# Kernel tuning notes

Hardware: AMD Instinct MI355X
Metric: run time of the kernel (lower is better)

Reference implementation:

```python
import jax, jax.numpy as jnp
import numpy as np

B, T, C = 2, 2048, 2048
N_HEAD = 16

def setup_inputs() -> dict:
    key = jax.random.key(0)
    k1, k2, k3 = jax.random.split(key, 3)
    scale = 1.0 / np.sqrt(C)
    return {
        "x": jax.random.normal(k1, (B, T, C), dtype=jnp.float32),
        "w_attn": jax.random.normal(k2, (C, 3 * C), dtype=jnp.float32) * scale,
        "b_attn": jnp.zeros((3 * C,), dtype=jnp.float32),
        "w_proj": jax.random.normal(k3, (C, C), dtype=jnp.float32) * scale,
        "b_proj": jnp.zeros((C,), dtype=jnp.float32),
    }

def reference(x, w_attn, b_attn, w_proj, b_proj):
    Bb, Tt, Cc = x.shape
    hd = Cc // N_HEAD  # head_size
    qkv = x @ w_attn + b_attn              # [B,T,3C]
    q, k, v = jnp.split(qkv, 3, axis=-1)
    # [B,T,C] -> [B,H,T,hd]
    def heads(t):
        return t.reshape(Bb, Tt, N_HEAD, hd).transpose(0, 2, 1, 3)
    q, k, v = heads(q), heads(k), heads(v)
    att = jnp.einsum("bhqd,bhkd->bhqk", q, k) * (hd ** -0.5)
    causal = jnp.tril(jnp.ones((Tt, Tt), dtype=bool))
    att = jnp.where(causal[None, None], att, -jnp.inf)
    att = jax.nn.softmax(att, axis=-1)
    out = jnp.einsum("bhqk,bhkd->bhqd", att, v)
    out = out.transpose(0, 2, 1, 3).reshape(Bb, Tt, Cc)
    return out @ w_proj + b_proj
```

## Files before the change

kernel.cpp:

```cpp
#include <hip/hip_runtime.h>
#include <cstdint>
#include <cstddef>

typedef __bf16 bf16_t;
typedef __bf16 bf16x8 __attribute__((ext_vector_type(8)));
typedef __bf16 bf16x4 __attribute__((ext_vector_type(4)));
typedef float floatx4 __attribute__((ext_vector_type(4)));
typedef float f32x16 __attribute__((ext_vector_type(16)));

#define B_  2
#define T_  2048
#define C_  2048
#define H_  16
#define HD_ 128

#define K_ATTN_SCALE (0.08838834764831843f * 1.44269504088896f)

__device__ __forceinline__ void async_copy16(const void* g, void* l) {
  __builtin_amdgcn_global_load_lds((const __attribute__((address_space(1))) unsigned int*)g,
                                   (__attribute__((address_space(3))) unsigned int*)l,
                                   16, 0, 0);
}

#define BAR()     asm volatile("s_barrier" ::: "memory")
#define VMCNT(n)  asm volatile("s_waitcnt vmcnt(" #n ")" ::: "memory")

__global__ __launch_bounds__(256) void cvt_f32_bf16(const float* __restrict__ in,
                                                    bf16_t* __restrict__ out, int n4) {
  int i = blockIdx.x * 256 + threadIdx.x;
  if (i >= n4) return;
  const float4 v = ((const float4*)in)[i];
  bf16x4 o;
  o[0] = (bf16_t)v.x; o[1] = (bf16_t)v.y; o[2] = (bf16_t)v.z; o[3] = (bf16_t)v.w;
  ((bf16x4*)out)[i] = o;
}

__global__ __launch_bounds__(256) void transpose_cvt(const float* __restrict__ W,
                                                     bf16_t* __restrict__ Wt,
                                                     int Kd, int Nd) {
  __shared__ float tile[32][33];
  const int tx = threadIdx.x, ty = threadIdx.y;
  const int n0 = blockIdx.x * 32, k0 = blockIdx.y * 32;
#pragma unroll
  for (int j = ty; j < 32; j += 8)
    tile[j][tx] = W[(size_t)(k0 + j) * Nd + n0 + tx];
  __syncthreads();
#pragma unroll
  for (int j = ty; j < 32; j += 8)
    Wt[(size_t)(n0 + j) * Kd + k0 + tx] = (bf16_t)tile[tx][j];
}

#define GBM 256
#define GBN 256
#define GBK 64

__global__ __launch_bounds__(512, 2) void gemm_qkv(
    const bf16_t* __restrict__ A, const bf16_t* __restrict__ Bt,
    const float* __restrict__ bias,
    bf16_t* __restrict__ Qo, bf16_t* __restrict__ Ko, bf16_t* __restrict__ Vo,
    int K) {
  __shared__ __align__(16) char smem[131072];
  const int tid = threadIdx.x;
  const int wave = tid >> 6, lane = tid & 63;
  const int quad = lane >> 4, l15 = lane & 15;
  const int wm = wave >> 2, wn = wave & 3;
  const int bm = blockIdx.y * GBM, bn = blockIdx.x * GBN;

  const bf16_t* asrc[2];
  const bf16_t* bsrc[2];
#pragma unroll
  for (int l = 0; l < 2; ++l) {
    int p = l * 8192 + tid * 16;
    int r = p >> 6;
    int c = ((p >> 4) & 3) ^ ((r >> 1) & 3);
    asrc[l] = A  + (size_t)(bm + r) * K + c * 8;
    bsrc[l] = Bt + (size_t)(bn + r) * K + c * 8;
  }

  auto stage = [&](int buf, int ks, int kofs) {
    char* Asl = smem + buf * 65536 + ks * 16384;
    char* Bsl = Asl + 32768;
#pragma unroll
    for (int l = 0; l < 2; ++l)
      async_copy16(asrc[l] + kofs, Asl + l * 8192 + tid * 16);
#pragma unroll
    for (int l = 0; l < 2; ++l)
      async_copy16(bsrc[l] + kofs, Bsl + l * 8192 + tid * 16);
  };

  const int sxr = ((l15 >> 1) & 3) << 4;
  const int cb  = (quad * 16) ^ sxr;
  const int arow = (wm * 128 + l15) * 64;
  const int brow = (wn * 64 + l15) * 64;

  floatx4 acc[8][4] = {};
  bf16x8 a0[4], a1[4], b0[4], b1[4];

  stage(0, 0, 0);
  stage(0, 1, 32);
  stage(1, 0, GBK);
  VMCNT(8);
  BAR();
  {
    const char* Ab = smem;
    const char* Bb = smem + 32768;
#pragma unroll
    for (int i = 0; i < 4; ++i)
      a0[i] = *(const bf16x8*)(Ab + arow + i * 1024 + cb);
#pragma unroll
    for (int j = 0; j < 4; ++j)
      b0[j] = *(const bf16x8*)(Bb + brow + j * 1024 + cb);
  }

  const int NT = K / GBK;
  for (int t = 0; t < NT; ++t) {
    const char* Ab  = smem + (t & 1) * 65536;
    const char* Bb  = Ab + 32768;
    const char* Abn = smem + ((t + 1) & 1) * 65536;
    const char* Bbn = Abn + 32768;

#pragma unroll
    for (int i = 0; i < 4; ++i)
      a1[i] = *(const bf16x8*)(Ab + arow + 4096 + i * 1024 + cb);
    if (t + 1 < NT) stage((t + 1) & 1, 1, (t + 1) * GBK + 32);
#pragma unroll
    for (int i = 0; i < 4; ++i)
#pragma unroll
      for (int j = 0; j < 4; ++j)
        acc[i][j] = __builtin_amdgcn_mfma_f32_16x16x32_bf16(a0[i], b0[j], acc[i][j], 0, 0, 0);
    if (t + 1 < NT) { VMCNT(8); } else { VMCNT(0); }
    BAR();

#pragma unroll
    for (int i = 0; i < 4; ++i)
      a0[i] = *(const bf16x8*)(Ab + 16384 + arow + i * 1024 + cb);
#pragma unroll
    for (int j = 0; j < 4; ++j)
      b1[j] = *(const bf16x8*)(Bb + 16384 + brow + j * 1024 + cb);
#pragma unroll
    for (int i = 0; i < 4; ++i)
#pragma unroll
      for (int j = 0; j < 4; ++j)
        acc[4 + i][j] = __builtin_amdgcn_mfma_f32_16x16x32_bf16(a1[i], b0[j], acc[4 + i][j], 0, 0, 0);

#pragma unroll
    for (int i = 0; i < 4; ++i)
      a1[i] = *(const bf16x8*)(Ab + 16384 + arow + 4096 + i * 1024 + cb);
    if (t + 2 < NT) stage(t & 1, 0, (t + 2) * GBK);
#pragma unroll
    for (int i = 0; i < 4; ++i)
#pragma unroll
      for (int j = 0; j < 4; ++j)
        acc[i][j] = __builtin_amdgcn_mfma_f32_16x16x32_bf16(a0[i], b1[j], acc[i][j], 0, 0, 0);
    if (t + 2 < NT)      { VMCNT(8); }
    else if (t + 1 < NT) { VMCNT(4); }
    else                 { VMCNT(0); }
    BAR();

    if (t + 1 < NT) {
#pragma unroll
      for (int i = 0; i < 4; ++i)
        a0[i] = *(const bf16x8*)(Abn + arow + i * 1024 + cb);
#pragma unroll
      for (int j = 0; j < 4; ++j)
        b0[j] = *(const bf16x8*)(Bbn + brow + j * 1024 + cb);
    }
#pragma unroll
    for (int i = 0; i < 4; ++i)
#pragma unroll
      for (int j = 0; j < 4; ++j)
        acc[4 + i][j] = __builtin_amdgcn_mfma_f32_16x16x32_bf16(a1[i], b1[j], acc[4 + i][j], 0, 0, 0);
  }

  float bias_r[4];
#pragma unroll
  for (int j = 0; j < 4; ++j)
    bias_r[j] = bias[bn + wn * 64 + j * 16 + l15];

  if (bn < 2 * C_) {
    const int which = bn >> 11;
    bf16_t* dst0 = which ? Ko : Qo;
    const float scl = which ? 1.0f : K_ATTN_SCALE;
#pragma unroll
    for (int i = 0; i < 8; ++i) {
      const int m = bm + wm * 128 + i * 16 + quad * 4;
      const int b = m >> 11, tq = m & 2047;
#pragma unroll
      for (int j = 0; j < 4; ++j) {
        const int n = bn + wn * 64 + j * 16 + l15;
        const int cc = n & 2047;
        const int h = cc >> 7, d = cc & 127;
        bf16_t* dst = dst0 + (((size_t)(b * H_ + h)) * T_ + tq) * HD_ + d;
#pragma unroll
        for (int r = 0; r < 4; ++r)
          dst[(size_t)r * HD_] = (bf16_t)((acc[i][j][r] + bias_r[j]) * scl);
      }
    }
  } else {
    __syncthreads();
    bf16_t* vt = (bf16_t*)smem;
#pragma unroll
    for (int i = 0; i < 8; ++i) {
      const int tl = wm * 128 + i * 16 + quad * 4;
#pragma unroll
      for (int j = 0; j < 4; ++j) {
        const int dl = wn * 64 + j * 16 + l15;
        const int sw = 8 * (dl & 15);
#pragma unroll
        for (int r = 0; r < 4; ++r)
          vt[dl * 256 + ((tl + r) ^ sw)] = (bf16_t)(acc[i][j][r] + bias_r[j]);
      }
    }
    __syncthreads();
    const int dr = tid >> 1, half = tid & 1;
    const int h = ((bn - 2 * C_) >> 7) + (dr >> 7);
    const int b = bm >> 11, t0g = bm & 2047;
    bf16_t* dst = Vo + ((size_t)(b * H_ + h) * HD_ + (dr & 127)) * T_ + t0g;
#pragma unroll
    for (int cc2 = 0; cc2 < 16; ++cc2) {
      const int c = half * 16 + cc2;
      uint4 v = *(const uint4*)&vt[dr * 256 + ((c ^ (dr & 15)) * 8)];
      *(uint4*)(dst + c * 8) = v;
    }
  }
}

#define TM 128
#define TN 128
#define BK 64

__global__ __launch_bounds__(256) void gemm_proj(
    const bf16_t* __restrict__ A, const bf16_t* __restrict__ Bt,
    const float* __restrict__ bias, float* __restrict__ Cout,
    int M, int N, int K) {
  __shared__ __align__(16) char smem[32768];
  bf16_t (*As)[BK] = (bf16_t(*)[BK])smem;
  bf16_t (*Bs)[BK] = (bf16_t(*)[BK])(smem + 16384);
  const int tid = threadIdx.x;
  const int wave = tid >> 6, lane = tid & 63;
  const int quad = lane >> 4, l15 = lane & 15;
  const int bm = blockIdx.y * TM, bn = blockIdx.x * TN;
  const int wm = (wave >> 1) * 64, wn = (wave & 1) * 64;
  const int sw = l15 & 7;

  floatx4 acc[4][4] = {};

  for (int k0 = 0; k0 < K; k0 += BK) {
#pragma unroll
    for (int it = 0; it < 4; ++it) {
      int p = it * 4096 + tid * 16;
      int r = p >> 7;
      int cg = ((p >> 4) & 7) ^ (r & 7);
      async_copy16(A + (size_t)(bm + r) * K + k0 + cg * 8, (char*)&As[0][0] + p);
      async_copy16(Bt + (size_t)(bn + r) * K + k0 + cg * 8, (char*)&Bs[0][0] + p);
    }
    __syncthreads();
#pragma unroll
    for (int kc = 0; kc < 2; ++kc) {
      const int cidx = (kc * 4 + quad) ^ sw;
      bf16x8 af[4], bf[4];
#pragma unroll
      for (int i = 0; i < 4; ++i)
        af[i] = *(const bf16x8*)&As[wm + i * 16 + l15][cidx * 8];
#pragma unroll
      for (int j = 0; j < 4; ++j)
        bf[j] = *(const bf16x8*)&Bs[wn + j * 16 + l15][cidx * 8];
#pragma unroll
      for (int i = 0; i < 4; ++i)
#pragma unroll
        for (int j = 0; j < 4; ++j)
          acc[i][j] = __builtin_amdgcn_mfma_f32_16x16x32_bf16(af[i], bf[j], acc[i][j], 0, 0, 0);
    }
    __syncthreads();
  }

#pragma unroll
  for (int i = 0; i < 4; ++i) {
#pragma unroll
    for (int j = 0; j < 4; ++j) {
#pragma unroll
      for (int r = 0; r < 4; ++r) {
        int m = bm + wm + i * 16 + quad * 4 + r;
        int n = bn + wn + j * 16 + l15;
        Cout[(size_t)m * N + n] = acc[i][j][r] + bias[n];
      }
    }
  }
}

__global__ __launch_bounds__(256) void attn(const bf16_t* __restrict__ Q,
                                            const bf16_t* __restrict__ Kg,
                                            const bf16_t* __restrict__ Vt,
                                            bf16_t* __restrict__ O) {
  __shared__ __align__(16) char smem[66560];
  const int tid = threadIdx.x;
  const int wave = tid >> 6, lane = tid & 63;
  const int hi = lane >> 5, l31 = lane & 31;
  const int qh = wave & 1, kh = wave >> 1;
  const int j = blockIdx.x;
  const int bh = blockIdx.y;
  const int b = bh >> 4, h = bh & 15;
  const int qtA = 31 - j, qtB = j;
  const int nchA = qtA + 1, nchB = qtB + 1;

  const bf16_t* Qh = Q + (size_t)bh * T_ * HD_;
  const bf16_t* Kh = Kg + (size_t)bh * T_ * HD_;
  const bf16_t* Vh = Vt + (size_t)bh * HD_ * T_;

  float* xb32 = (float*)smem;
  float* lbuf = (float*)(smem + 65536);

  auto stage = [&](int buf, int kt0) {
#pragma unroll
    for (int it = 0; it < 4; ++it) {
      int p = it * 4096 + tid * 16;
      int r = p >> 8;
      int cg = ((p >> 4) & 15) ^ (r & 15);
      async_copy16(Kh + (size_t)(kt0 + r) * HD_ + cg * 8, smem + buf * 16384 + p);
    }
#pragma unroll
    for (int it = 0; it < 4; ++it) {
      int p = it * 4096 + tid * 16;
      int r = p >> 7;
      int cg = ((p >> 4) & 7) ^ (r & 7);
      async_copy16(Vh + (size_t)r * T_ + kt0 + cg * 8, smem + 32768 + buf * 16384 + p);
    }
  };

  const int q0Arow = qtA * 64 + qh * 32;
  const int q0Brow = qtB * 64 + qh * 32;
  const bf16_t* qpA = Qh + (size_t)(q0Arow + l31) * HD_ + hi * 8;
  const bf16_t* qpB = Qh + (size_t)(q0Brow + l31) * HD_ + hi * 8;

  f32x16 oA[4] = {}, oB[4] = {};
  float l_A = 0.0f, l_B = 0.0f;

  const int swk = l31 & 15;
  const int swv = l31 & 7;
  const int krbase = (kh * 32 + l31) * 256;

  auto slot = [&](int buf, int kt0, const bf16_t* qp, f32x16 (&oacc)[4], float& l_i,
                  int qrow, bool mask) {
    const char* Kb = smem + buf * 16384;
    const char* Vb = smem + 32768 + buf * 16384;
    f32x16 s0 = {}, s1 = {};
#pragma unroll
    for (int m = 0; m < 4; ++m) {
      bf16x8 kf = *(const bf16x8*)(Kb + krbase + (((2 * m + hi) ^ swk) << 4));
      bf16x8 qf = *(const bf16x8*)(qp + m * 16);
      s0 = __builtin_amdgcn_mfma_f32_32x32x16_bf16(kf, qf, s0, 0, 0, 0);
    }
#pragma unroll
    for (int m = 4; m < 8; ++m) {
      bf16x8 kf = *(const bf16x8*)(Kb + krbase + (((2 * m + hi) ^ swk) << 4));
      bf16x8 qf = *(const bf16x8*)(qp + m * 16);
      s1 = __builtin_amdgcn_mfma_f32_32x32x16_bf16(kf, qf, s1, 0, 0, 0);
    }
    const int qg = qrow + l31;
    float p[16];
    float ps = 0.0f;
#pragma unroll
    for (int r = 0; r < 16; ++r) {
      float v = s0[r] + s1[r];
      float e = __builtin_amdgcn_exp2f(v);
      if (mask) {
        int kt = kt0 + kh * 32 + (r & 3) + 8 * (r >> 2) + 4 * hi;
        e = (kt <= qg) ? e : 0.0f;
      }
      ps += e;
      p[r] = e;
    }
    ps += __shfl_xor(ps, 32);
    l_i += ps;
    union PF { unsigned int w[4]; bf16x8 v; } pf[2];
#pragma unroll
    for (int m2 = 0; m2 < 2; ++m2) {
      union PK { bf16_t h[2]; unsigned int u; } a0, a1, c0, c1;
      const int ga = 8 * m2, gb = 8 * m2 + 4;
      a0.h[0] = (bf16_t)p[ga + 0]; a0.h[1] = (bf16_t)p[ga + 1];
      a1.h[0] = (bf16_t)p[ga + 2]; a1.h[1] = (bf16_t)p[ga + 3];
      c0.h[0] = (bf16_t)p[gb + 0]; c0.h[1] = (bf16_t)p[gb + 1];
      c1.h[0] = (bf16_t)p[gb + 2]; c1.h[1] = (bf16_t)p[gb + 3];
      unsigned int wa0 = a0.u, wa1 = a1.u, wb0 = c0.u, wb1 = c1.u;
      asm("v_permlane32_swap_b32 %0, %1" : "+v"(wa0), "+v"(wb0));
      asm("v_permlane32_swap_b32 %0, %1" : "+v"(wa1), "+v"(wb1));
      pf[m2].w[0] = wa0; pf[m2].w[1] = wa1; pf[m2].w[2] = wb0; pf[m2].w[3] = wb1;
    }
#pragma unroll
    for (int g = 0; g < 4; ++g) {
      const int vrb = (g * 32 + l31) * 128;
#pragma unroll
      for (int m2 = 0; m2 < 2; ++m2) {
        const int cc = kh * 4 + m2 * 2 + hi;
        bf16x8 vf = *(const bf16x8*)(Vb + vrb + ((cc ^ swv) << 4));
        oacc[g] = __builtin_amdgcn_mfma_f32_32x32x16_bf16(vf, pf[m2].v, oacc[g], 0, 0, 0);
      }
    }
  };

  stage(0, 0);
  for (int ch = 0; ch < nchA; ++ch) {
    __syncthreads();
    if (ch + 1 < nchA) stage((ch + 1) & 1, (ch + 1) * 64);
    const int buf = ch & 1;
    slot(buf, ch * 64, qpA, oA, l_A, q0Arow, ch == nchA - 1);
    if (ch < nchB)
      slot(buf, ch * 64, qpB, oB, l_B, q0Brow, ch == nchB - 1);
  }

  auto dumpAcc = [&](f32x16 (&o)[4], float lp) {
#pragma unroll
    for (int g = 0; g < 4; ++g)
#pragma unroll
      for (int r = 0; r < 16; ++r)
        xb32[qh * 4096 + (g * 16 + r) * 64 + lane] = o[g][r];
    lbuf[qh * 64 + lane] = lp;
  };
  auto combineTile = [&](f32x16 (&o)[4], float lp) {
    const float inv = 1.0f / (lp + lbuf[qh * 64 + lane]);
    const int rr = qh * 32 + l31;
    char* ob = smem + 32768 + rr * 256;
#pragma unroll
    for (int g = 0; g < 4; ++g)
#pragma unroll
      for (int r1 = 0; r1 < 4; ++r1) {
        union { bf16_t hh[4]; uint2 u2; } w;
#pragma unroll
        for (int k = 0; k < 4; ++k)
          w.hh[k] = (bf16_t)((o[g][r1 * 4 + k] +
                              xb32[qh * 4096 + (g * 16 + r1 * 4 + k) * 64 + lane]) * inv);
        const int chunk = 4 * g + r1;
        *(uint2*)(ob + ((chunk ^ (rr & 15)) << 4) + 8 * hi) = w.u2;
      }
  };
  auto storeTile = [&](int qt) {
    const int row = tid >> 2, seg = tid & 3;
    bf16_t* Og = O + ((size_t)(b * T_ + qt * 64 + row)) * C_ + h * HD_;
    const char* sb = smem + 32768 + row * 256;
#pragma unroll
    for (int c4 = 0; c4 < 4; ++c4) {
      const int c = seg * 4 + c4;
      uint4 v = *(const uint4*)(sb + ((c ^ (row & 15)) << 4));
      *(uint4*)(Og + c * 8) = v;
    }
  };

  __syncthreads();
  if (wave >= 2) dumpAcc(oA, l_A);
  __syncthreads();
  if (wave < 2) combineTile(oA, l_A);
  __syncthreads();
  storeTile(qtA);
  if (wave >= 2) dumpAcc(oB, l_B);
  __syncthreads();
  if (wave < 2) combineTile(oB, l_B);
  __syncthreads();
  storeTile(qtB);
}

extern "C" void kernel_launch(void* const* d_in, const int* in_sizes, int n_in,
                              void* d_out, int out_size, void* d_ws, size_t ws_size,
                              hipStream_t stream) {
  const float* x      = (const float*)d_in[0];
  const float* w_attn = (const float*)d_in[1];
  const float* b_attn = (const float*)d_in[2];
  const float* w_proj = (const float*)d_in[3];
  const float* b_proj = (const float*)d_in[4];
  float* out = (float*)d_out;

  char* p = (char*)d_ws;
  bf16_t* xb  = (bf16_t*)p; p += (size_t)4096 * 2048 * 2;
  bf16_t* waT = (bf16_t*)p; p += (size_t)6144 * 2048 * 2;
  bf16_t* wpT = (bf16_t*)p; p += (size_t)2048 * 2048 * 2;
  bf16_t* Qb  = (bf16_t*)p; p += (size_t)32 * 2048 * 128 * 2;
  bf16_t* Kb  = (bf16_t*)p; p += (size_t)32 * 2048 * 128 * 2;
  bf16_t* Vb  = (bf16_t*)p; p += (size_t)32 * 2048 * 128 * 2;
  bf16_t* Ob  = (bf16_t*)p; p += (size_t)4096 * 2048 * 2;

  cvt_f32_bf16<<<8192, 256, 0, stream>>>(x, xb, 2097152);
  transpose_cvt<<<dim3(6144 / 32, 2048 / 32), dim3(32, 8), 0, stream>>>(w_attn, waT, 2048, 6144);
  transpose_cvt<<<dim3(2048 / 32, 2048 / 32), dim3(32, 8), 0, stream>>>(w_proj, wpT, 2048, 2048);

  gemm_qkv<<<dim3(6144 / GBN, 4096 / GBM), 512, 0, stream>>>(
      xb, waT, b_attn, Qb, Kb, Vb, 2048);

  attn<<<dim3(16, 32), 256, 0, stream>>>(Qb, Kb, Vb, Ob);

  gemm_proj<<<dim3(2048 / TN, 4096 / TM), 256, 0, stream>>>(
      Ob, wpT, b_proj, out, 4096, 2048, 2048);
}
```

Before: 412.3 us.

## Unify QKV and projection GEMMs into a templated 256x128 pipelined kernel

Shrinks the QKV GEMM tile from 256x256 to 256x128 (8 waves arranged 4x2, each computing 64x64) and restructures the k-loop into two half-steps with one barrier each. The V-transpose epilogue is reworked for the narrower tile with a new LDS swizzle. The separate 128x128 projection GEMM is replaced by the same pipelined kernel in a float-output mode. This aims to improve grid fill (more blocks on 256 CUs) and to give the projection the double-buffered async pipeline, at the cost of lower arithmetic intensity per block for the QKV GEMM.

```diff
diff --git a/kernel.cpp b/kernel.cpp
--- a/kernel.cpp
+++ b/kernel.cpp
@@ -51,55 +51,58 @@
 }
 
 #define GBM 256
-#define GBN 256
+#define GBN 128
 #define GBK 64
 
-__global__ __launch_bounds__(512, 2) void gemm_qkv(
+template <int MODE>
+__global__ __launch_bounds__(512, 2) void gemm256(
     const bf16_t* __restrict__ A, const bf16_t* __restrict__ Bt,
-    const float* __restrict__ bias,
+    const float* __restrict__ bias, float* __restrict__ Cout,
     bf16_t* __restrict__ Qo, bf16_t* __restrict__ Ko, bf16_t* __restrict__ Vo,
-    int K) {
-  __shared__ __align__(16) char smem[131072];
+    int N, int K) {
+  __shared__ __align__(16) char smem[98304];
   const int tid = threadIdx.x;
   const int wave = tid >> 6, lane = tid & 63;
   const int quad = lane >> 4, l15 = lane & 15;
-  const int wm = wave >> 2, wn = wave & 3;
+  const int wm = wave >> 1, wn = wave & 1;
   const int bm = blockIdx.y * GBM, bn = blockIdx.x * GBN;
 
   const bf16_t* asrc[2];
-  const bf16_t* bsrc[2];
+  const bf16_t* bsrc;
 #pragma unroll
   for (int l = 0; l < 2; ++l) {
     int p = l * 8192 + tid * 16;
     int r = p >> 6;
     int c = ((p >> 4) & 3) ^ ((r >> 1) & 3);
-    asrc[l] = A  + (size_t)(bm + r) * K + c * 8;
-    bsrc[l] = Bt + (size_t)(bn + r) * K + c * 8;
+    asrc[l] = A + (size_t)(bm + r) * K + c * 8;
+  }
+  {
+    int p = tid * 16;
+    int r = p >> 6;
+    int c = ((p >> 4) & 3) ^ ((r >> 1) & 3);
+    bsrc = Bt + (size_t)(bn + r) * K + c * 8;
   }
 
   auto stage = [&](int buf, int ks, int kofs) {
-    char* Asl = smem + buf * 65536 + ks * 16384;
-    char* Bsl = Asl + 32768;
-#pragma unroll
-    for (int l = 0; l < 2; ++l)
-      async_copy16(asrc[l] + kofs, Asl + l * 8192 + tid * 16);
-#pragma unroll
-    for (int l = 0; l < 2; ++l)
-      async_copy16(bsrc[l] + kofs, Bsl + l * 8192 + tid * 16);
+    char* Asl = smem + buf * 49152 + ks * 16384;
+    char* Bsl = smem + buf * 49152 + 32768 + ks * 8192;
+    async_copy16(asrc[0] + kofs, Asl + tid * 16);
+    async_copy16(asrc[1] + kofs, Asl + 8192 + tid * 16);
+    async_copy16(bsrc + kofs, Bsl + tid * 16);
   };
 
   const int sxr = ((l15 >> 1) & 3) << 4;
   const int cb  = (quad * 16) ^ sxr;
-  const int arow = (wm * 128 + l15) * 64;
+  const int arow = (wm * 64 + l15) * 64;
   const int brow = (wn * 64 + l15) * 64;
 
-  floatx4 acc[8][4] = {};
+  floatx4 acc[4][4] = {};
   bf16x8 a0[4], a1[4], b0[4], b1[4];
 
   stage(0, 0, 0);
   stage(0, 1, 32);
   stage(1, 0, GBK);
-  VMCNT(8);
+  VMCNT(3);
   BAR();
   {
     const char* Ab = smem;
@@ -114,47 +117,24 @@
 
   const int NT = K / GBK;
   for (int t = 0; t < NT; ++t) {
-    const char* Ab  = smem + (t & 1) * 65536;
+    const char* Ab  = smem + (t & 1) * 49152;
     const char* Bb  = Ab + 32768;
-    const char* Abn = smem + ((t + 1) & 1) * 65536;
+    const char* Abn = smem + ((t + 1) & 1) * 49152;
     const char* Bbn = Abn + 32768;
 
 #pragma unroll
     for (int i = 0; i < 4; ++i)
-      a1[i] = *(const bf16x8*)(Ab + arow + 4096 + i * 1024 + cb);
+      a1[i] = *(const bf16x8*)(Ab + 16384 + arow + i * 1024 + cb);
+#pragma unroll
+    for (int j = 0; j < 4; ++j)
+      b1[j] = *(const bf16x8*)(Bb + 8192 + brow + j * 1024 + cb);
     if (t + 1 < NT) stage((t + 1) & 1, 1, (t + 1) * GBK + 32);
 #pragma unroll
     for (int i = 0; i < 4; ++i)
 #pragma unroll
       for (int j = 0; j < 4; ++j)
         acc[i][j] = __builtin_amdgcn_mfma_f32_16x16x32_bf16(a0[i], b0[j], acc[i][j], 0, 0, 0);
-    if (t + 1 < NT) { VMCNT(8); } else { VMCNT(0); }
-    BAR();
-
-#pragma unroll
-    for (int i = 0; i < 4; ++i)
-      a0[i] = *(const bf16x8*)(Ab + 16384 + arow + i * 1024 + cb);
-#pragma unroll
-    for (int j = 0; j < 4; ++j)
-      b1[j] = *(const bf16x8*)(Bb + 16384 + brow + j * 1024 + cb);
-#pragma unroll
-    for (int i = 0; i < 4; ++i)
-#pragma unroll
-      for (int j = 0; j < 4; ++j)
-        acc[4 + i][j] = __builtin_amdgcn_mfma_f32_16x16x32_bf16(a1[i], b0[j], acc[4 + i][j], 0, 0, 0);
-
-#pragma unroll
-    for (int i = 0; i < 4; ++i)
-      a1[i] = *(const bf16x8*)(Ab + 16384 + arow + 4096 + i * 1024 + cb);
-    if (t + 2 < NT) stage(t & 1, 0, (t + 2) * GBK);
-#pragma unroll
-    for (int i = 0; i < 4; ++i)
-#pragma unroll
-      for (int j = 0; j < 4; ++j)
-        acc[i][j] = __builtin_amdgcn_mfma_f32_16x16x32_bf16(a0[i], b1[j], acc[i][j], 0, 0, 0);
-    if (t + 2 < NT)      { VMCNT(8); }
-    else if (t + 1 < NT) { VMCNT(4); }
-    else                 { VMCNT(0); }
+    if (t + 1 < NT) { VMCNT(3); }
     BAR();
 
     if (t + 1 < NT) {
@@ -165,25 +145,45 @@
       for (int j = 0; j < 4; ++j)
         b0[j] = *(const bf16x8*)(Bbn + brow + j * 1024 + cb);
     }
+    if (t + 2 < NT) stage(t & 1, 0, (t + 2) * GBK);
 #pragma unroll
     for (int i = 0; i < 4; ++i)
 #pragma unroll
       for (int j = 0; j < 4; ++j)
-        acc[4 + i][j] = __builtin_amdgcn_mfma_f32_16x16x32_bf16(a1[i], b1[j], acc[4 + i][j], 0, 0, 0);
+        acc[i][j] = __builtin_amdgcn_mfma_f32_16x16x32_bf16(a1[i], b1[j], acc[i][j], 0, 0, 0);
+    if (t + 2 < NT)      { VMCNT(3); }
+    else if (t + 1 < NT) { VMCNT(0); }
+    BAR();
   }
 
   float bias_r[4];
 #pragma unroll
   for (int j = 0; j < 4; ++j)
     bias_r[j] = bias[bn + wn * 64 + j * 16 + l15];
+
+  if (MODE == 1) {
+#pragma unroll
+    for (int i = 0; i < 4; ++i) {
+#pragma unroll
+      for (int j = 0; j < 4; ++j) {
+#pragma unroll
+        for (int r = 0; r < 4; ++r) {
+          int m = bm + wm * 64 + i * 16 + quad * 4 + r;
+          int n = bn + wn * 64 + j * 16 + l15;
+          Cout[(size_t)m * N + n] = acc[i][j][r] + bias_r[j];
+        }
+      }
+    }
+    return;
+  }
 
   if (bn < 2 * C_) {
     const int which = bn >> 11;
     bf16_t* dst0 = which ? Ko : Qo;
     const float scl = which ? 1.0f : K_ATTN_SCALE;
 #pragma unroll
-    for (int i = 0; i < 8; ++i) {
-      const int m = bm + wm * 128 + i * 16 + quad * 4;
+    for (int i = 0; i < 4; ++i) {
+      const int m = bm + wm * 64 + i * 16 + quad * 4;
       const int b = m >> 11, tq = m & 2047;
 #pragma unroll
       for (int j = 0; j < 4; ++j) {
@@ -200,90 +200,30 @@
     __syncthreads();
     bf16_t* vt = (bf16_t*)smem;
 #pragma unroll
-    for (int i = 0; i < 8; ++i) {
-      const int tl = wm * 128 + i * 16 + quad * 4;
+    for (int i = 0; i < 4; ++i) {
+      const int tl0 = wm * 64 + i * 16 + quad * 4;
 #pragma unroll
       for (int j = 0; j < 4; ++j) {
         const int dl = wn * 64 + j * 16 + l15;
-        const int sw = 8 * (dl & 15);
-#pragma unroll
-        for (int r = 0; r < 4; ++r)
-          vt[dl * 256 + ((tl + r) ^ sw)] = (bf16_t)(acc[i][j][r] + bias_r[j]);
+        const int sw = dl & 31;
+#pragma unroll
+        for (int r = 0; r < 4; ++r) {
+          const int tl = tl0 + r;
+          vt[dl * 256 + ((((tl >> 3) ^ sw) << 3) + (tl & 7))] =
+              (bf16_t)(acc[i][j][r] + bias_r[j]);
+        }
       }
     }
     __syncthreads();
-    const int dr = tid >> 1, half = tid & 1;
-    const int h = ((bn - 2 * C_) >> 7) + (dr >> 7);
+    const int d = tid >> 2, seg = tid & 3;
+    const int h = (bn - 2 * C_) >> 7;
     const int b = bm >> 11, t0g = bm & 2047;
-    bf16_t* dst = Vo + ((size_t)(b * H_ + h) * HD_ + (dr & 127)) * T_ + t0g;
-#pragma unroll
-    for (int cc2 = 0; cc2 < 16; ++cc2) {
-      const int c = half * 16 + cc2;
-      uint4 v = *(const uint4*)&vt[dr * 256 + ((c ^ (dr & 15)) * 8)];
-      *(uint4*)(dst + c * 8) = v;
-    }
-  }
-}
-
-#define TM 128
-#define TN 128
-#define BK 64
-
-__global__ __launch_bounds__(256) void gemm_proj(
-    const bf16_t* __restrict__ A, const bf16_t* __restrict__ Bt,
-    const float* __restrict__ bias, float* __restrict__ Cout,
-    int M, int N, int K) {
-  __shared__ __align__(16) char smem[32768];
-  bf16_t (*As)[BK] = (bf16_t(*)[BK])smem;
-  bf16_t (*Bs)[BK] = (bf16_t(*)[BK])(smem + 16384);
-  const int tid = threadIdx.x;
-  const int wave = tid >> 6, lane = tid & 63;
-  const int quad = lane >> 4, l15 = lane & 15;
-  const int bm = blockIdx.y * TM, bn = blockIdx.x * TN;
-  const int wm = (wave >> 1) * 64, wn = (wave & 1) * 64;
-  const int sw = l15 & 7;
-
-  floatx4 acc[4][4] = {};
-
-  for (int k0 = 0; k0 < K; k0 += BK) {
-#pragma unroll
-    for (int it = 0; it < 4; ++it) {
-      int p = it * 4096 + tid * 16;
-      int r = p >> 7;
-      int cg = ((p >> 4) & 7) ^ (r & 7);
-      async_copy16(A + (size_t)(bm + r) * K + k0 + cg * 8, (char*)&As[0][0] + p);
-      async_copy16(Bt + (size_t)(bn + r) * K + k0 + cg * 8, (char*)&Bs[0][0] + p);
-    }
-    __syncthreads();
-#pragma unroll
-    for (int kc = 0; kc < 2; ++kc) {
-      const int cidx = (kc * 4 + quad) ^ sw;
-      bf16x8 af[4], bf[4];
-#pragma unroll
-      for (int i = 0; i < 4; ++i)
-        af[i] = *(const bf16x8*)&As[wm + i * 16 + l15][cidx * 8];
-#pragma unroll
-      for (int j = 0; j < 4; ++j)
-        bf[j] = *(const bf16x8*)&Bs[wn + j * 16 + l15][cidx * 8];
-#pragma unroll
-      for (int i = 0; i < 4; ++i)
-#pragma unroll
-        for (int j = 0; j < 4; ++j)
-          acc[i][j] = __builtin_amdgcn_mfma_f32_16x16x32_bf16(af[i], bf[j], acc[i][j], 0, 0, 0);
-    }
-    __syncthreads();
-  }
-
-#pragma unroll
-  for (int i = 0; i < 4; ++i) {
-#pragma unroll
-    for (int j = 0; j < 4; ++j) {
-#pragma unroll
-      for (int r = 0; r < 4; ++r) {
-        int m = bm + wm + i * 16 + quad * 4 + r;
-        int n = bn + wn + j * 16 + l15;
-        Cout[(size_t)m * N + n] = acc[i][j][r] + bias[n];
-      }
+    bf16_t* dst = Vo + ((size_t)(b * H_ + h) * HD_ + d) * T_ + t0g;
+#pragma unroll
+    for (int c8 = 0; c8 < 8; ++c8) {
+      const int chunk = seg * 8 + c8;
+      uint4 v = *(const uint4*)&vt[d * 256 + ((chunk ^ (d & 31)) << 3)];
+      *(uint4*)(dst + chunk * 8) = v;
     }
   }
 }
@@ -481,11 +421,11 @@
   transpose_cvt<<<dim3(6144 / 32, 2048 / 32), dim3(32, 8), 0, stream>>>(w_attn, waT, 2048, 6144);
   transpose_cvt<<<dim3(2048 / 32, 2048 / 32), dim3(32, 8), 0, stream>>>(w_proj, wpT, 2048, 2048);
 
-  gemm_qkv<<<dim3(6144 / GBN, 4096 / GBM), 512, 0, stream>>>(
-      xb, waT, b_attn, Qb, Kb, Vb, 2048);
+  gemm256<0><<<dim3(6144 / GBN, 4096 / GBM), 512, 0, stream>>>(
+      xb, waT, b_attn, nullptr, Qb, Kb, Vb, 6144, 2048);
 
   attn<<<dim3(16, 32), 256, 0, stream>>>(Qb, Kb, Vb, Ob);
 
-  gemm_proj<<<dim3(2048 / TN, 4096 / TM), 256, 0, stream>>>(
-      Ob, wpT, b_proj, out, 4096, 2048, 2048);
-}
+  gemm256<1><<<dim3(2048 / GBN, 4096 / GBM), 512, 0, stream>>>(
+      Ob, wpT, b_proj, out, nullptr, nullptr, nullptr, 2048, 2048);
+}
```

Result: faster. 389.6 us (-5.5%).
